# Kernel optimization log

Measured on AMD Instinct MI355X. Metric: run time of the kernel, lower is better.

Reference implementation:

```python
import math
import jax, jax.numpy as jnp
import numpy as np

KERNEL_SIZES = [3, 5, 7, 9, 11, 13, 15, 17]
NUM_HEADS = 2
EMBED = len(KERNEL_SIZES)  # 8
HEAD_DIM = EMBED // NUM_HEADS  # 4


def _moving_avg(x2, k):
    # x2: [B, S]; replicate-pad so output length == S (MovingAvg padding scheme)
    front = k - 1 - (k - 1) // 2
    end = (k - 1) // 2
    p = jnp.concatenate([
        jnp.repeat(x2[:, :1], front, axis=1), x2,
        jnp.repeat(x2[:, -1:], end, axis=1)
    ], axis=1)  # [B, S+k-1]
    w = jnp.full((1, 1, k), 1.0 / k, dtype=x2.dtype)
    y = jax.lax.conv_general_dilated(p[:, None, :], w, (1,), 'VALID')
    return y[:, 0, :]  # [B, S]


def setup_inputs() -> dict:
    key = jax.random.key(0)
    ks = jax.random.split(key, 6)
    B, S = 32, 2048
    D, E = HEAD_DIM, EMBED
    sd = 1.0 / math.sqrt(D)
    x = jax.random.normal(ks[0], (B, S, 1), dtype=jnp.float32)
    Wq = jax.random.normal(ks[1], (D, D), dtype=jnp.float32) * sd
    Wk = jax.random.normal(ks[2], (D, D), dtype=jnp.float32) * sd
    Wv = jax.random.normal(ks[3], (D, D), dtype=jnp.float32) * sd
    Wo = jax.random.normal(ks[4], (E, E), dtype=jnp.float32) * (1.0 / math.sqrt(E))
    bo = jax.random.normal(ks[5], (E,), dtype=jnp.float32) * 0.01
    return {"x": x, "Wq": Wq, "Wk": Wk, "Wv": Wv, "Wo": Wo, "bo": bo}


def reference(x, Wq, Wk, Wv, Wo, bo):
    B, S, _ = x.shape
    H, D, E = NUM_HEADS, HEAD_DIM, EMBED
    x2 = x[..., 0]  # [B, S]
    # multi moving-average branches -> concat on channel dim
    mm = jnp.stack([_moving_avg(x2, k) for k in KERNEL_SIZES], axis=-1)  # [B,S,E]
    t = mm.reshape(B, S, H, D)
    # nn.Linear(head_dim, head_dim, bias=False): y = x @ W^T (shared across heads)
    q = jnp.einsum('bshd,ed->bshe', t, Wq)
    k_ = jnp.einsum('bshd,ed->bshe', t, Wk)
    v = jnp.einsum('bshd,ed->bshe', t, Wv)
    scale = jnp.asarray(math.sqrt(D), dtype=x.dtype)
    energy = jnp.einsum('bqhd,bkhd->bhqk', q, k_) / scale  # [B,H,S,S]
    att = jax.nn.softmax(energy, axis=-1)  # dropout is identity in eval mode
    o = jnp.einsum('bhqk,bkhd->bqhd', att, v).reshape(B, S, E)
    o = o @ Wo.T + bo  # fc_out
    weights = jax.nn.softmax(o, axis=-1)  # [B,S,E]
    trend = jnp.sum(mm * weights, axis=-1, keepdims=True)  # [B,S,1]
    seasonal = x - trend
    return seasonal, trend
```

## Files before the change

### kernel.cpp

```cpp
#include <hip/hip_runtime.h>

#define SB 32
#define SS 2048
#define SH 2
#define SD 4
#define SE 8

#define LOG2E 1.44269504f

typedef float    f32x16 __attribute__((ext_vector_type(16)));
typedef _Float16 f16x8  __attribute__((ext_vector_type(8)));

static __device__ __forceinline__ float fast_exp2(float x) {
#if __has_builtin(__builtin_amdgcn_exp2f)
    return __builtin_amdgcn_exp2f(x);
#else
    return exp2f(x);
#endif
}

static __device__ __forceinline__ int cvtpk(float a, float b) {
    auto h = __builtin_amdgcn_cvt_pkrtz(a, b);
    union { decltype(h) hh; int i; } u; u.hh = h; return u.i;
}

static __device__ __forceinline__ void swap32(int a, int b, int lane, int& r0, int& r1) {
#if __has_builtin(__builtin_amdgcn_permlane32_swap)
    auto r = __builtin_amdgcn_permlane32_swap(a, b, false, false);
    r0 = r[0]; r1 = r[1];
#else
    const int blo = __builtin_amdgcn_ds_bpermute((lane & 31) << 2, b);
    const int ahi = __builtin_amdgcn_ds_bpermute(((lane ^ 32) & 63) << 2, a);
    r0 = (lane < 32) ? a : blo;
    r1 = (lane < 32) ? ahi : b;
#endif
}

static __device__ __forceinline__ f16x8 frag2(unsigned x, unsigned y) {
    union { unsigned u[4]; f16x8 h; } c;
    c.u[0] = x; c.u[1] = y; c.u[2] = 0; c.u[3] = 0; return c.h;
}
static __device__ __forceinline__ f16x8 frag4(uint4 v) {
    union { uint4 u; f16x8 h; } c; c.u = v; return c.h;
}
static __device__ __forceinline__ f16x8 fragi(int a, int b, int c_, int d) {
    union { int u[4]; f16x8 h; } c;
    c.u[0] = a; c.u[1] = b; c.u[2] = c_; c.u[3] = d; return c.h;
}

union u32h2 { unsigned u; _Float16 h[2]; };
static __device__ __forceinline__ unsigned packh2(float a, float b) {
    u32h2 c; c.h[0] = (_Float16)a; c.h[1] = (_Float16)b; return c.u;
}

__global__ __launch_bounds__(256) void k_ma_qkv(
    const float* __restrict__ x,
    const float* __restrict__ Wq,
    const float* __restrict__ Wk,
    const float* __restrict__ Wv,
    uint2* __restrict__ qws16,
    uint2* __restrict__ kws16,
    _Float16* __restrict__ vtg,
    float4* __restrict__ mmws)
{
    __shared__ float xs[272];

    const int tile = blockIdx.x % (SS / 256);
    const int b    = blockIdx.x / (SS / 256);
    const int s0   = tile * 256;
    const float* xrow = x + b * SS;

    for (int i = threadIdx.x; i < 272; i += 256) {
        int idx = s0 - 8 + i;
        idx = min(max(idx, 0), SS - 1);
        xs[i] = xrow[idx];
    }
    __syncthreads();

    const int t = threadIdx.x;
    const int s = s0 + t;

    float mmv[8];
    float c = xs[8 + t];
    #pragma unroll
    for (int h = 1; h <= 8; ++h) {
        c += xs[8 + t - h] + xs[8 + t + h];
        mmv[h - 1] = c * (1.0f / (float)(2 * h + 1));
    }

    mmws[(b * SS + s) * 2 + 0] = make_float4(mmv[0], mmv[1], mmv[2], mmv[3]);
    mmws[(b * SS + s) * 2 + 1] = make_float4(mmv[4], mmv[5], mmv[6], mmv[7]);

    const float qscale = 0.5f * LOG2E;
    #pragma unroll
    for (int h = 0; h < SH; ++h) {
        const float t0 = mmv[h * 4 + 0];
        const float t1 = mmv[h * 4 + 1];
        const float t2 = mmv[h * 4 + 2];
        const float t3 = mmv[h * 4 + 3];
        float q[4], k[4], v[4];
        #pragma unroll
        for (int e = 0; e < 4; ++e) {
            q[e] = (t0 * Wq[e * 4 + 0] + t1 * Wq[e * 4 + 1] +
                    t2 * Wq[e * 4 + 2] + t3 * Wq[e * 4 + 3]) * qscale;
            k[e] =  t0 * Wk[e * 4 + 0] + t1 * Wk[e * 4 + 1] +
                    t2 * Wk[e * 4 + 2] + t3 * Wk[e * 4 + 3];
            v[e] =  t0 * Wv[e * 4 + 0] + t1 * Wv[e * 4 + 1] +
                    t2 * Wv[e * 4 + 2] + t3 * Wv[e * 4 + 3];
        }
        const int bh  = b * SH + h;
        const int idx = bh * SS + s;
        qws16[idx] = make_uint2(packh2(q[0], q[1]), packh2(q[2], q[3]));
        kws16[idx] = make_uint2(packh2(k[0], k[1]), packh2(k[2], k[3]));
        #pragma unroll
        for (int e = 0; e < 4; ++e)
            vtg[(bh * 4 + e) * SS + s] = (_Float16)v[e];
    }
}

#define LDS_K    0
#define LDS_VT   16384
#define VT_STRIDE 4112
#define LDS_Z    36944
#define LDS_SIZE 37376

__global__ __launch_bounds__(256) void k_attn(
    const uint2* __restrict__ qws16,
    const uint2* __restrict__ kws16,
    const unsigned* __restrict__ vtg,
    float4* __restrict__ ows)
{
    __shared__ __align__(16) char lds[LDS_SIZE];

    const int t      = threadIdx.x;
    const int bh     = blockIdx.x >> 4;
    const int w      = t >> 6;
    const int iblock = (blockIdx.x & 15) * 4 + w;
    const int lane   = t & 63;
    const int c31    = lane & 31;

    const uint2* kg = kws16 + bh * SS;
    for (int i = t; i < SS; i += 256)
        *(uint2*)(lds + LDS_K + i * 8) = kg[i];
    const unsigned* vg = vtg + bh * 4 * (SS / 2);
    for (int i = t; i < 4 * (SS / 2); i += 256) {
        const int cc = i >> 10, col = i & 1023;
        *(unsigned*)(lds + LDS_VT + cc * VT_STRIDE + col * 4) = vg[i];
    }
    for (int i = t; i < SS / 2; i += 256)
        *(unsigned*)(lds + LDS_VT + 4 * VT_STRIDE + i * 4) = 0x3C003C00u;
    if (t < 32) *(unsigned*)(lds + LDS_Z + t * 4) = 0u;
    __syncthreads();

    uint2 qq = qws16[bh * SS + iblock * 32 + c31];
    if (lane >= 32) { qq.x = 0u; qq.y = 0u; }
    const f16x8 bq = frag2(qq.x, qq.y);

    int kaddr = (lane < 32) ? (LDS_K + lane * 8) : LDS_Z;
    const int kstep = (lane < 32) ? 256 : 0;
    int vaddr = (c31 < 5) ? (LDS_VT + c31 * VT_STRIDE + (lane >> 5) * 16) : LDS_Z;
    const int vstep = (c31 < 5) ? 64 : 0;

    f32x16 oacc = {0,0,0,0,0,0,0,0,0,0,0,0,0,0,0,0};
    const f32x16 zc = {0,0,0,0,0,0,0,0,0,0,0,0,0,0,0,0};

    uint2 kk = *(const uint2*)(lds + kaddr); kaddr += kstep;
    uint4 vv0 = *(const uint4*)(lds + vaddr);
    uint4 vv1 = *(const uint4*)(lds + vaddr + 32); vaddr += vstep;
    f32x16 d_cur = __builtin_amdgcn_mfma_f32_32x32x16_f16(frag2(kk.x, kk.y), bq, zc, 0, 0, 0);
    kk = *(const uint2*)(lds + kaddr); kaddr += kstep;

    #pragma unroll 2
    for (int jt = 0; jt < SS / 32; ++jt) {
        const f16x8 av0 = frag4(vv0);
        const f16x8 av1 = frag4(vv1);

        f32x16 d_next = __builtin_amdgcn_mfma_f32_32x32x16_f16(frag2(kk.x, kk.y), bq, zc, 0, 0, 0);

        kk  = *(const uint2*)(lds + kaddr); kaddr += kstep;
        vv0 = *(const uint4*)(lds + vaddr);
        vv1 = *(const uint4*)(lds + vaddr + 32); vaddr += vstep;

        float p[16];
        #pragma unroll
        for (int r = 0; r < 16; ++r) p[r] = fast_exp2(d_cur[r]);

        const int pk01 = cvtpk(p[0],  p[1]),  pk23 = cvtpk(p[2],  p[3]);
        const int pk45 = cvtpk(p[4],  p[5]),  pk67 = cvtpk(p[6],  p[7]);
        const int pk89 = cvtpk(p[8],  p[9]),  pkAB = cvtpk(p[10], p[11]);
        const int pkCD = cvtpk(p[12], p[13]), pkEF = cvtpk(p[14], p[15]);

        int B0, B1, B2, B3, C0, C1, C2, C3;
        swap32(pk01, pk45, lane, B0, B2);
        swap32(pk23, pk67, lane, B1, B3);
        swap32(pk89, pkCD, lane, C0, C2);
        swap32(pkAB, pkEF, lane, C1, C3);

        const f16x8 bp0 = fragi(B0, B1, B2, B3);
        const f16x8 bp1 = fragi(C0, C1, C2, C3);

        oacc = __builtin_amdgcn_mfma_f32_32x32x16_f16(av0, bp0, oacc, 0, 0, 0);
        oacc = __builtin_amdgcn_mfma_f32_32x32x16_f16(av1, bp1, oacc, 0, 0, 0);

        d_cur = d_next;
    }

    union { float f; int i; } u0; u0.f = oacc[0];
    int s0i, s1i;
    swap32(u0.i, u0.i, lane, s0i, s1i);
    union { int i; float f; } ul; ul.i = s1i;
    if (lane < 32) {
        const float inv = 1.0f / ul.f;
        ows[bh * SS + iblock * 32 + lane] =
            make_float4(oacc[0] * inv, oacc[1] * inv, oacc[2] * inv, oacc[3] * inv);
    }
}

__global__ __launch_bounds__(256) void k_epilogue(
    const float* __restrict__ x,
    const float* __restrict__ Wo,
    const float* __restrict__ bo,
    const float4* __restrict__ ows,
    const float4* __restrict__ mmws,
    float* __restrict__ out)
{
    const int pos = blockIdx.x * 256 + threadIdx.x;
    const int b = pos / SS;
    const int s = pos % SS;

    const float4 o0 = ows[(b * SH + 0) * SS + s];
    const float4 o1 = ows[(b * SH + 1) * SS + s];
    const float ov[8] = {o0.x, o0.y, o0.z, o0.w, o1.x, o1.y, o1.z, o1.w};

    float g[8];
    float m = -1e30f;
    #pragma unroll
    for (int e = 0; e < 8; ++e) {
        float acc = bo[e];
        #pragma unroll
        for (int f = 0; f < 8; ++f) acc += ov[f] * Wo[e * 8 + f];
        g[e] = acc;
        m = fmaxf(m, acc);
    }
    float l = 0.0f;
    #pragma unroll
    for (int e = 0; e < 8; ++e) { g[e] = __expf(g[e] - m); l += g[e]; }
    const float inv = 1.0f / l;

    const float4 mm0 = mmws[pos * 2 + 0];
    const float4 mm1 = mmws[pos * 2 + 1];
    const float mv[8] = {mm0.x, mm0.y, mm0.z, mm0.w, mm1.x, mm1.y, mm1.z, mm1.w};

    float trend = 0.0f;
    #pragma unroll
    for (int e = 0; e < 8; ++e) trend += g[e] * inv * mv[e];

    out[pos]           = x[pos] - trend;
    out[SB * SS + pos] = trend;
}

extern "C" void kernel_launch(void* const* d_in, const int* in_sizes, int n_in,
                              void* d_out, int out_size, void* d_ws, size_t ws_size,
                              hipStream_t stream) {
    const float* x  = (const float*)d_in[0];
    const float* Wq = (const float*)d_in[1];
    const float* Wk = (const float*)d_in[2];
    const float* Wv = (const float*)d_in[3];
    const float* Wo = (const float*)d_in[4];
    const float* bo = (const float*)d_in[5];

    uint2*     qws16 = (uint2*)d_ws;
    uint2*     kws16 = qws16 + SB * SH * SS;
    _Float16*  vtg   = (_Float16*)(kws16 + SB * SH * SS);
    float4*    mmws  = (float4*)(vtg + SB * SH * 4 * SS);
    float4*    ows   = mmws + SB * SS * 2;

    k_ma_qkv<<<SB * (SS / 256), 256, 0, stream>>>(x, Wq, Wk, Wv, qws16, kws16, vtg, mmws);
    k_attn<<<SB * SH * 16, 256, 0, stream>>>(qws16, kws16, (const unsigned*)vtg, ows);
    k_epilogue<<<(SB * SS) / 256, 256, 0, stream>>>(x, Wo, bo, ows, mmws, (float*)d_out);
}
```

Before: 50.75 us.

## Process two query tiles per wave to reuse K/V loads and interleave MFMAs

Each wave in the attention kernel now handles two 32-row query blocks, so every K and V fragment read from LDS feeds two sets of QK and PV MFMAs. The grid is halved, which also halves the per-block staging of K and V into LDS. The QK product uses the smaller 32x32x8 f16 MFMA when the compiler provides it, and the PV MFMAs are wrapped in s_setprio to favour the matrix pipe. The explicit unroll pragma is dropped. The cost is more registers per wave (two accumulators and two score tiles) and fewer blocks, which may reduce occupancy and latency hiding.

```diff
diff --git a/kernel.cpp b/kernel.cpp
--- a/kernel.cpp
+++ b/kernel.cpp
@@ -10,6 +10,7 @@
 
 typedef float    f32x16 __attribute__((ext_vector_type(16)));
 typedef _Float16 f16x8  __attribute__((ext_vector_type(8)));
+typedef _Float16 f16x4  __attribute__((ext_vector_type(4)));
 
 static __device__ __forceinline__ float fast_exp2(float x) {
 #if __has_builtin(__builtin_amdgcn_exp2f)
@@ -47,6 +48,24 @@
     union { int u[4]; f16x8 h; } c;
     c.u[0] = a; c.u[1] = b; c.u[2] = c_; c.u[3] = d; return c.h;
 }
+
+#if __has_builtin(__builtin_amdgcn_mfma_f32_32x32x8f16)
+typedef f16x4 qkfrag;
+static __device__ __forceinline__ qkfrag make_qk(unsigned x, unsigned y) {
+    union { unsigned u[2]; f16x4 h; } c; c.u[0] = x; c.u[1] = y; return c.h;
+}
+static __device__ __forceinline__ f32x16 qk_mfma(qkfrag a, qkfrag b, f32x16 c) {
+    return __builtin_amdgcn_mfma_f32_32x32x8f16(a, b, c, 0, 0, 0);
+}
+#else
+typedef f16x8 qkfrag;
+static __device__ __forceinline__ qkfrag make_qk(unsigned x, unsigned y) {
+    return frag2(x, y);
+}
+static __device__ __forceinline__ f32x16 qk_mfma(qkfrag a, qkfrag b, f32x16 c) {
+    return __builtin_amdgcn_mfma_f32_32x32x16_f16(a, b, c, 0, 0, 0);
+}
+#endif
 
 union u32h2 { unsigned u; _Float16 h[2]; };
 static __device__ __forceinline__ unsigned packh2(float a, float b) {
@@ -123,8 +142,9 @@
 #define VT_STRIDE 4112
 #define LDS_Z    36944
 #define LDS_SIZE 37376
-
-__global__ __launch_bounds__(256) void k_attn(
+#define NT       (SS / 32)
+
+__global__ __launch_bounds__(256, 2) void k_attn(
     const uint2* __restrict__ qws16,
     const uint2* __restrict__ kws16,
     const unsigned* __restrict__ vtg,
@@ -132,12 +152,14 @@
 {
     __shared__ __align__(16) char lds[LDS_SIZE];
 
-    const int t      = threadIdx.x;
-    const int bh     = blockIdx.x >> 4;
-    const int w      = t >> 6;
-    const int iblock = (blockIdx.x & 15) * 4 + w;
-    const int lane   = t & 63;
-    const int c31    = lane & 31;
+    const int t    = threadIdx.x;
+    const int bh   = blockIdx.x >> 3;
+    const int part = blockIdx.x & 7;
+    const int w    = t >> 6;
+    const int ib0  = part * 8 + w;
+    const int ib1  = ib0 + 4;
+    const int lane = t & 63;
+    const int c31  = lane & 31;
 
     const uint2* kg = kws16 + bh * SS;
     for (int i = t; i < SS; i += 256)
@@ -152,67 +174,102 @@
     if (t < 32) *(unsigned*)(lds + LDS_Z + t * 4) = 0u;
     __syncthreads();
 
-    uint2 qq = qws16[bh * SS + iblock * 32 + c31];
-    if (lane >= 32) { qq.x = 0u; qq.y = 0u; }
-    const f16x8 bq = frag2(qq.x, qq.y);
+    uint2 qq0 = qws16[bh * SS + ib0 * 32 + c31];
+    uint2 qq1 = qws16[bh * SS + ib1 * 32 + c31];
+    if (lane >= 32) { qq0.x = 0u; qq0.y = 0u; qq1.x = 0u; qq1.y = 0u; }
+    const qkfrag bq0 = make_qk(qq0.x, qq0.y);
+    const qkfrag bq1 = make_qk(qq1.x, qq1.y);
 
     int kaddr = (lane < 32) ? (LDS_K + lane * 8) : LDS_Z;
     const int kstep = (lane < 32) ? 256 : 0;
     int vaddr = (c31 < 5) ? (LDS_VT + c31 * VT_STRIDE + (lane >> 5) * 16) : LDS_Z;
     const int vstep = (c31 < 5) ? 64 : 0;
 
-    f32x16 oacc = {0,0,0,0,0,0,0,0,0,0,0,0,0,0,0,0};
+    f32x16 oacc0 = {0,0,0,0,0,0,0,0,0,0,0,0,0,0,0,0};
+    f32x16 oacc1 = {0,0,0,0,0,0,0,0,0,0,0,0,0,0,0,0};
     const f32x16 zc = {0,0,0,0,0,0,0,0,0,0,0,0,0,0,0,0};
 
     uint2 kk = *(const uint2*)(lds + kaddr); kaddr += kstep;
+    f32x16 d0 = qk_mfma(make_qk(kk.x, kk.y), bq0, zc);
+    f32x16 d1 = qk_mfma(make_qk(kk.x, kk.y), bq1, zc);
+    kk = *(const uint2*)(lds + kaddr); kaddr += kstep;
     uint4 vv0 = *(const uint4*)(lds + vaddr);
     uint4 vv1 = *(const uint4*)(lds + vaddr + 32); vaddr += vstep;
-    f32x16 d_cur = __builtin_amdgcn_mfma_f32_32x32x16_f16(frag2(kk.x, kk.y), bq, zc, 0, 0, 0);
-    kk = *(const uint2*)(lds + kaddr); kaddr += kstep;
-
-    #pragma unroll 2
-    for (int jt = 0; jt < SS / 32; ++jt) {
-        const f16x8 av0 = frag4(vv0);
-        const f16x8 av1 = frag4(vv1);
-
-        f32x16 d_next = __builtin_amdgcn_mfma_f32_32x32x16_f16(frag2(kk.x, kk.y), bq, zc, 0, 0, 0);
-
-        kk  = *(const uint2*)(lds + kaddr); kaddr += kstep;
-        vv0 = *(const uint4*)(lds + vaddr);
-        vv1 = *(const uint4*)(lds + vaddr + 32); vaddr += vstep;
+
+    for (int jt = 0; jt < NT; ++jt) {
+        const qkfrag ak = make_qk(kk.x, kk.y);
 
         float p[16];
         #pragma unroll
-        for (int r = 0; r < 16; ++r) p[r] = fast_exp2(d_cur[r]);
-
-        const int pk01 = cvtpk(p[0],  p[1]),  pk23 = cvtpk(p[2],  p[3]);
-        const int pk45 = cvtpk(p[4],  p[5]),  pk67 = cvtpk(p[6],  p[7]);
-        const int pk89 = cvtpk(p[8],  p[9]),  pkAB = cvtpk(p[10], p[11]);
-        const int pkCD = cvtpk(p[12], p[13]), pkEF = cvtpk(p[14], p[15]);
-
-        int B0, B1, B2, B3, C0, C1, C2, C3;
-        swap32(pk01, pk45, lane, B0, B2);
-        swap32(pk23, pk67, lane, B1, B3);
-        swap32(pk89, pkCD, lane, C0, C2);
-        swap32(pkAB, pkEF, lane, C1, C3);
-
-        const f16x8 bp0 = fragi(B0, B1, B2, B3);
-        const f16x8 bp1 = fragi(C0, C1, C2, C3);
-
-        oacc = __builtin_amdgcn_mfma_f32_32x32x16_f16(av0, bp0, oacc, 0, 0, 0);
-        oacc = __builtin_amdgcn_mfma_f32_32x32x16_f16(av1, bp1, oacc, 0, 0, 0);
-
-        d_cur = d_next;
-    }
-
-    union { float f; int i; } u0; u0.f = oacc[0];
-    int s0i, s1i;
-    swap32(u0.i, u0.i, lane, s0i, s1i);
-    union { int i; float f; } ul; ul.i = s1i;
-    if (lane < 32) {
-        const float inv = 1.0f / ul.f;
-        ows[bh * SS + iblock * 32 + lane] =
-            make_float4(oacc[0] * inv, oacc[1] * inv, oacc[2] * inv, oacc[3] * inv);
+        for (int r = 0; r < 16; ++r) p[r] = fast_exp2(d0[r]);
+        int F00, F01, F02, F03;
+        {
+            const int pk01 = cvtpk(p[0],  p[1]),  pk23 = cvtpk(p[2],  p[3]);
+            const int pk45 = cvtpk(p[4],  p[5]),  pk67 = cvtpk(p[6],  p[7]);
+            const int pk89 = cvtpk(p[8],  p[9]),  pkAB = cvtpk(p[10], p[11]);
+            const int pkCD = cvtpk(p[12], p[13]), pkEF = cvtpk(p[14], p[15]);
+            int B0, B1, B2, B3, C0, C1, C2, C3;
+            swap32(pk01, pk45, lane, B0, B2);
+            swap32(pk23, pk67, lane, B1, B3);
+            swap32(pk89, pkCD, lane, C0, C2);
+            swap32(pkAB, pkEF, lane, C1, C3);
+            F00 = B0; F01 = B1; F02 = B2; F03 = B3;
+            d0 = qk_mfma(ak, bq0, zc);
+            const f16x8 bpC = fragi(C0, C1, C2, C3);
+            const f16x8 av0 = frag4(vv0);
+            const f16x8 av1 = frag4(vv1);
+            __builtin_amdgcn_s_setprio(1);
+            oacc0 = __builtin_amdgcn_mfma_f32_32x32x16_f16(av0, fragi(F00, F01, F02, F03), oacc0, 0, 0, 0);
+            oacc0 = __builtin_amdgcn_mfma_f32_32x32x16_f16(av1, bpC, oacc0, 0, 0, 0);
+            __builtin_amdgcn_s_setprio(0);
+        }
+
+        #pragma unroll
+        for (int r = 0; r < 16; ++r) p[r] = fast_exp2(d1[r]);
+        {
+            const int pk01 = cvtpk(p[0],  p[1]),  pk23 = cvtpk(p[2],  p[3]);
+            const int pk45 = cvtpk(p[4],  p[5]),  pk67 = cvtpk(p[6],  p[7]);
+            const int pk89 = cvtpk(p[8],  p[9]),  pkAB = cvtpk(p[10], p[11]);
+            const int pkCD = cvtpk(p[12], p[13]), pkEF = cvtpk(p[14], p[15]);
+            int B0, B1, B2, B3, C0, C1, C2, C3;
+            swap32(pk01, pk45, lane, B0, B2);
+            swap32(pk23, pk67, lane, B1, B3);
+            swap32(pk89, pkCD, lane, C0, C2);
+            swap32(pkAB, pkEF, lane, C1, C3);
+            d1 = qk_mfma(ak, bq1, zc);
+            const f16x8 av0 = frag4(vv0);
+            const f16x8 av1 = frag4(vv1);
+            kk  = *(const uint2*)(lds + kaddr); kaddr += kstep;
+            vv0 = *(const uint4*)(lds + vaddr);
+            vv1 = *(const uint4*)(lds + vaddr + 32); vaddr += vstep;
+            __builtin_amdgcn_s_setprio(1);
+            oacc1 = __builtin_amdgcn_mfma_f32_32x32x16_f16(av0, fragi(B0, B1, B2, B3), oacc1, 0, 0, 0);
+            oacc1 = __builtin_amdgcn_mfma_f32_32x32x16_f16(av1, fragi(C0, C1, C2, C3), oacc1, 0, 0, 0);
+            __builtin_amdgcn_s_setprio(0);
+        }
+    }
+
+    {
+        union { float f; int i; } u0; u0.f = oacc0[0];
+        int s0i, s1i;
+        swap32(u0.i, u0.i, lane, s0i, s1i);
+        union { int i; float f; } ul; ul.i = s1i;
+        if (lane < 32) {
+            const float inv = 1.0f / ul.f;
+            ows[bh * SS + ib0 * 32 + lane] =
+                make_float4(oacc0[0] * inv, oacc0[1] * inv, oacc0[2] * inv, oacc0[3] * inv);
+        }
+    }
+    {
+        union { float f; int i; } u0; u0.f = oacc1[0];
+        int s0i, s1i;
+        swap32(u0.i, u0.i, lane, s0i, s1i);
+        union { int i; float f; } ul; ul.i = s1i;
+        if (lane < 32) {
+            const float inv = 1.0f / ul.f;
+            ows[bh * SS + ib1 * 32 + lane] =
+                make_float4(oacc1[0] * inv, oacc1[1] * inv, oacc1[2] * inv, oacc1[3] * inv);
+        }
     }
 }
 
@@ -276,6 +333,6 @@
     float4*    ows   = mmws + SB * SS * 2;
 
     k_ma_qkv<<<SB * (SS / 256), 256, 0, stream>>>(x, Wq, Wk, Wv, qws16, kws16, vtg, mmws);
-    k_attn<<<SB * SH * 16, 256, 0, stream>>>(qws16, kws16, (const unsigned*)vtg, ows);
+    k_attn<<<SB * SH * 8, 256, 0, stream>>>(qws16, kws16, (const unsigned*)vtg, ows);
     k_epilogue<<<(SB * SS) / 256, 256, 0, stream>>>(x, Wo, bo, ows, mmws, (float*)d_out);
 }
```

New measurement: 44.97 us. -11.4%, faster.
